# Performance work log

Measured on AMD Instinct MI355X. Metric: run time of the kernel, lower is better.

The kernel has to match this reference:

```python
import jax, jax.numpy as jnp
import numpy as np

B, S, E = 2, 2048, 1024
H, D = 16, 64
BASE = 10000.0


def rotate_half(x):
    x1, x2 = jnp.split(x, 2, axis=-1)
    return jnp.concatenate((-x2, x1), axis=-1)


def rope_cos_sin(seq_len, dim):
    inv_freq = 1.0 / (BASE ** (jnp.arange(0, dim, 2, dtype=jnp.float32) / dim))
    t = jnp.arange(seq_len, dtype=jnp.float32)
    freqs = jnp.einsum('i,j->ij', t, inv_freq)          # [S, D/2]
    emb = jnp.concatenate((freqs, freqs), axis=-1)       # [S, D]
    return jnp.cos(emb), jnp.sin(emb)


def setup_inputs() -> dict:
    key = jax.random.key(0)
    ks = jax.random.split(key, 9)
    s = 1.0 / np.sqrt(E)
    inp = {
        'x': jax.random.normal(ks[0], (B, S, E), dtype=jnp.float32),
        'mask': jnp.ones((B, S), dtype=jnp.int32),
        'Wq': jax.random.normal(ks[1], (E, H * D), dtype=jnp.float32) * s,
        'bq': jnp.zeros((H * D,), dtype=jnp.float32),
        'Wk': jax.random.normal(ks[2], (E, H * D), dtype=jnp.float32) * s,
        'bk': jnp.zeros((H * D,), dtype=jnp.float32),
        'Wv': jax.random.normal(ks[3], (E, H * D), dtype=jnp.float32) * s,
        'bv': jnp.zeros((H * D,), dtype=jnp.float32),
        'Wo': jax.random.normal(ks[4], (H * D, E), dtype=jnp.float32) * s,
        'bo': jnp.zeros((E,), dtype=jnp.float32),
    }
    return inp


def reference(x, mask, Wq, bq, Wk, bk, Wv, bv, Wo, bo):
    b, s, _ = x.shape
    scale = D ** (-0.5)
    # projections -> [B, H, S, D]
    q = (x @ Wq + bq).reshape(b, s, H, D).transpose(0, 2, 1, 3)
    k = (x @ Wk + bk).reshape(b, s, H, D).transpose(0, 2, 1, 3)
    v = (x @ Wv + bv).reshape(b, s, H, D).transpose(0, 2, 1, 3)
    # rotary position embedding
    cos, sin = rope_cos_sin(s, D)                      # [S, D]
    cos = cos[None, None]
    sin = sin[None, None]
    q = q * cos + rotate_half(q) * sin
    k = k * cos + rotate_half(k) * sin
    # scores [B, H, S, S]
    scores = jnp.einsum('bhqd,bhkd->bhqk', q, k) * scale
    # padding mask [B,1,1,S]
    scores = jnp.where(mask[:, None, None, :] == 0, -jnp.inf, scores)
    # causal mask
    i = jnp.arange(s)
    causal = jnp.where(i[None, :] > i[:, None], -jnp.inf, 0.0)  # [S, S]
    scores = scores + causal[None, None]
    attn = jax.nn.softmax(scores, axis=-1)
    ctx = jnp.einsum('bhqk,bhkd->bhqd', attn, v)
    ctx = ctx.transpose(0, 2, 1, 3).reshape(b, s, H * D)
    return ctx @ Wo + bo
```

## Files before the change

### kernel.cpp

```cpp
#include <hip/hip_runtime.h>
#include <cstdint>
#include <cstddef>

#define DEVI __device__ __forceinline__

typedef __bf16 bf16_t;
typedef __bf16 bf16x4 __attribute__((ext_vector_type(4)));
typedef __bf16 bf16x8 __attribute__((ext_vector_type(8)));
typedef float  f32x4  __attribute__((ext_vector_type(4)));
typedef float  f32x16 __attribute__((ext_vector_type(16)));
typedef unsigned short u16x4 __attribute__((ext_vector_type(4)));
typedef unsigned int   u32x4 __attribute__((ext_vector_type(4)));

static constexpr int Bz = 2, S = 2048, E = 1024, H = 16, Dh = 64;
static constexpr int M  = Bz * S;
static constexpr int N  = H * Dh;
static constexpr int Kd = E;

DEVI unsigned short f2bf(float f) {
  unsigned u = __builtin_bit_cast(unsigned, f);
  return (unsigned short)((u + 0x7fffu + ((u >> 16) & 1u)) >> 16);
}

DEVI void async_copy16(void* lds, const void* g) {
  __builtin_amdgcn_global_load_lds((__attribute__((address_space(1))) void*)(g),
                                   (__attribute__((address_space(3))) void*)(lds), 16, 0, 0);
}

DEVI void block_sync() { asm volatile("s_barrier" ::: "memory"); }
#define VMCNT4() asm volatile("s_waitcnt vmcnt(4)" ::: "memory")
#define VMCNT0() asm volatile("s_waitcnt vmcnt(0)" ::: "memory")

DEVI unsigned cvtpk(float lo, float hi) {
  unsigned r;
  asm("v_cvt_pk_bf16_f32 %0, %1, %2" : "=v"(r) : "v"(lo), "v"(hi));
  return r;
}
DEVI void swap32(unsigned& x, unsigned& y) {
  asm("v_permlane32_swap_b32 %0, %1" : "+v"(x), "+v"(y));
}

__global__ void prep_kernel(const float* __restrict__ x, bf16_t* __restrict__ xb,
                            const float* __restrict__ Wq, const float* __restrict__ Wk,
                            const float* __restrict__ Wv, const float* __restrict__ Wo,
                            bf16_t* __restrict__ WtBase,
                            float* __restrict__ ropeC, float* __restrict__ ropeS) {
  __shared__ unsigned short tile[64][68];
  const int blk = blockIdx.x, tid = threadIdx.x;
  if (blk < 4096) {
    int i = blk * 256 + tid;
    float4 v = ((const float4*)x)[i];
    u16x4 o = { f2bf(v.x), f2bf(v.y), f2bf(v.z), f2bf(v.w) };
    ((u16x4*)xb)[i] = o;
  } else if (blk < 5120) {
    const int i = blk - 4096;
    const int z = i >> 8, rest = i & 255;
    const int n0 = (rest & 15) * 64, k0 = (rest >> 4) * 64;
    const float* W = (z == 0) ? Wq : (z == 1) ? Wk : (z == 2) ? Wv : Wo;
    unsigned short* T = (unsigned short*)(WtBase + (size_t)z * Kd * N);
    for (int e = tid; e < 1024; e += 256) {
      int r = e >> 4, c4 = (e & 15) * 4;
      float4 v = *(const float4*)(W + (size_t)(k0 + r) * N + n0 + c4);
      u16x4 o = { f2bf(v.x), f2bf(v.y), f2bf(v.z), f2bf(v.w) };
      *(u16x4*)&tile[r][c4] = o;
    }
    __syncthreads();
    for (int e = tid; e < 1024; e += 256) {
      int r = e >> 4, c4 = (e & 15) * 4;
      u16x4 o = { tile[c4][r], tile[c4 + 1][r], tile[c4 + 2][r], tile[c4 + 3][r] };
      *(u16x4*)&T[(size_t)(n0 + r) * Kd + k0 + c4] = o;
    }
  } else {
    int i = (blk - 5120) * 256 + tid;
    int pos = i >> 5, j = i & 31;
    float inv = exp2f(-(float)j * 0.41524101186092029f);
    float ang = (float)pos * inv;
    ropeC[i] = cosf(ang);
    ropeS[i] = sinf(ang);
  }
}

__global__ void vtrans_kernel(const bf16_t* __restrict__ V, bf16_t* __restrict__ Vt) {
  __shared__ unsigned short tile[64][68];
  const int bh = blockIdx.y;
  const int s0 = blockIdx.x * 64;
  const unsigned short* Vp = (const unsigned short*)V + (size_t)bh * S * Dh;
  unsigned short* Tp = (unsigned short*)Vt + (size_t)bh * Dh * S;
  const int tid = threadIdx.x;
  for (int e = tid; e < 1024; e += 256) {
    int r = e >> 4, c4 = (e & 15) * 4;
    u16x4 v = *(const u16x4*)(Vp + (size_t)(s0 + r) * Dh + c4);
    *(u16x4*)&tile[r][c4] = v;
  }
  __syncthreads();
  for (int e = tid; e < 1024; e += 256) {
    int d = e >> 4, s4 = (e & 15) * 4;
    u16x4 o = { tile[s4][d], tile[s4 + 1][d], tile[s4 + 2][d], tile[s4 + 3][d] };
    *(u16x4*)&Tp[(size_t)d * S + s0 + s4] = o;
  }
}


DEVI void gemm_mainloop(const bf16_t* __restrict__ A, const bf16_t* __restrict__ Bt,
                        bf16_t* sA, bf16_t* sB, int m0, int n0, f32x4 (&acc)[4][4]) {
  const int tid  = threadIdx.x;
  const int lane = tid & 63;
  const int wid  = tid >> 6;
  const int l16  = lane & 15;
  const int quad = lane >> 4;
  const int wm = (wid >> 1) * 64;
  const int wn = (wid & 1) * 64;
  const int o0 = wid * 2048 + lane * 16;
  const int o1 = o0 + 1024;
  const int r0 = o0 >> 6, c0 = o0 & 63;
  const int r1 = o1 >> 6, c1 = o1 & 63;
  const char* Ab = (const char*)A;
  const char* Bb = (const char*)Bt;
  char* sAc = (char*)sA;
  char* sBc = (char*)sB;

  for (int k0 = 0; k0 < Kd; k0 += 32) {
    __syncthreads();
    async_copy16(sAc + wid * 2048,        Ab + ((size_t)(m0 + r0) * Kd + k0) * 2 + c0);
    async_copy16(sAc + wid * 2048 + 1024, Ab + ((size_t)(m0 + r1) * Kd + k0) * 2 + c1);
    async_copy16(sBc + wid * 2048,        Bb + ((size_t)(n0 + r0) * Kd + k0) * 2 + c0);
    async_copy16(sBc + wid * 2048 + 1024, Bb + ((size_t)(n0 + r1) * Kd + k0) * 2 + c1);
    __syncthreads();
    bf16x8 af[4], bfv[4];
#pragma unroll
    for (int mi = 0; mi < 4; ++mi)
      af[mi] = *(const bf16x8*)(sA + (wm + mi * 16 + l16) * 32 + quad * 8);
#pragma unroll
    for (int ni = 0; ni < 4; ++ni)
      bfv[ni] = *(const bf16x8*)(sB + (wn + ni * 16 + l16) * 32 + quad * 8);
#pragma unroll
    for (int mi = 0; mi < 4; ++mi)
#pragma unroll
      for (int ni = 0; ni < 4; ++ni)
        acc[mi][ni] = __builtin_amdgcn_mfma_f32_16x16x32_bf16(af[mi], bfv[ni], acc[mi][ni], 0, 0, 0);
  }
}

__global__ __launch_bounds__(256, 3) void gemm_qkv_kernel(
    const bf16_t* __restrict__ xb, const bf16_t* __restrict__ WtBase,
    const float* __restrict__ bq, const float* __restrict__ bk, const float* __restrict__ bv,
    bf16_t* __restrict__ outBase,
    const float* __restrict__ ropeC, const float* __restrict__ ropeS) {
  __shared__ bf16_t sA[4096], sB[4096];
  const int z = blockIdx.z;
  const bf16_t* Bt = WtBase + (size_t)z * Kd * N;
  const float* bias = (z == 0) ? bq : (z == 1) ? bk : bv;
  unsigned short* outp = (unsigned short*)(outBase + (size_t)z * M * N);
  const int n0 = blockIdx.x * 128, m0 = blockIdx.y * 128;
  f32x4 acc[4][4] = {};
  gemm_mainloop(xb, Bt, sA, sB, m0, n0, acc);

  const int tid = threadIdx.x, lane = tid & 63, wid = tid >> 6;
  const int l16 = lane & 15, quad = lane >> 4;
  const int wm = (wid >> 1) * 64, wn = (wid & 1) * 64;
  const int cbase = n0 + wn;
  const int h = cbase >> 6;

  if (z < 2) {
    const float qs = (z == 0) ? 0.18033688011112042f : 1.0f;
#pragma unroll
    for (int mi = 0; mi < 4; ++mi)
#pragma unroll
      for (int r = 0; r < 4; ++r) {
        int t = m0 + wm + mi * 16 + quad * 4 + r;
        int bb = t >> 11, s = t & (S - 1);
        size_t obase = ((size_t)(bb * H + h) * S + s) * Dh;
#pragma unroll
        for (int np = 0; np < 2; ++np) {
          int j = np * 16 + l16;
          float cc = ropeC[s * 32 + j];
          float ss = ropeS[s * 32 + j];
          float xlo = acc[mi][np][r]     + bias[cbase + j];
          float xhi = acc[mi][np + 2][r] + bias[cbase + j + 32];
          outp[obase + j]      = f2bf((xlo * cc - xhi * ss) * qs);
          outp[obase + j + 32] = f2bf((xhi * cc + xlo * ss) * qs);
        }
      }
  } else {
#pragma unroll
    for (int mi = 0; mi < 4; ++mi)
#pragma unroll
      for (int r = 0; r < 4; ++r) {
        int t = m0 + wm + mi * 16 + quad * 4 + r;
        int bb = t >> 11, s = t & (S - 1);
        size_t obase = ((size_t)(bb * H + h) * S + s) * Dh;
#pragma unroll
        for (int ni = 0; ni < 4; ++ni) {
          int d = ni * 16 + l16;
          outp[obase + d] = f2bf(acc[mi][ni][r] + bias[cbase + d]);
        }
      }
  }
}

__global__ __launch_bounds__(256, 4) void gemm_o_kernel(
    const bf16_t* __restrict__ A, const bf16_t* __restrict__ Bt,
    const float* __restrict__ bias, float* __restrict__ out) {
  __shared__ bf16_t sA[2048], sB[4096];
  const int n0 = blockIdx.x * 128, m0 = blockIdx.y * 64;
  const int tid = threadIdx.x, lane = tid & 63, wid = tid >> 6;
  const int l16 = lane & 15, quad = lane >> 4;
  const int wm = (wid >> 1) * 32, wn = (wid & 1) * 64;
  const int rowoff = lane >> 2, col8 = (lane & 3) * 8;
  const char* Ab = (const char*)A;
  const char* Bb = (const char*)Bt;
  char* sAc = (char*)sA;
  char* sBc = (char*)sB;
  f32x4 acc[2][4] = {};

  for (int k0 = 0; k0 < Kd; k0 += 32) {
    __syncthreads();
    async_copy16(sAc + wid * 1024,
                 Ab + ((size_t)(m0 + wid * 16 + rowoff) * Kd + k0 + col8) * 2);
    async_copy16(sBc + (wid * 2) * 1024,
                 Bb + ((size_t)(n0 + wid * 32 + rowoff) * Kd + k0 + col8) * 2);
    async_copy16(sBc + (wid * 2 + 1) * 1024,
                 Bb + ((size_t)(n0 + wid * 32 + 16 + rowoff) * Kd + k0 + col8) * 2);
    __syncthreads();
    bf16x8 af[2], bfv[4];
#pragma unroll
    for (int mi = 0; mi < 2; ++mi)
      af[mi] = *(const bf16x8*)(sA + (wm + mi * 16 + l16) * 32 + quad * 8);
#pragma unroll
    for (int ni = 0; ni < 4; ++ni)
      bfv[ni] = *(const bf16x8*)(sB + (wn + ni * 16 + l16) * 32 + quad * 8);
#pragma unroll
    for (int mi = 0; mi < 2; ++mi)
#pragma unroll
      for (int ni = 0; ni < 4; ++ni)
        acc[mi][ni] = __builtin_amdgcn_mfma_f32_16x16x32_bf16(af[mi], bfv[ni], acc[mi][ni], 0, 0, 0);
  }
#pragma unroll
  for (int mi = 0; mi < 2; ++mi)
#pragma unroll
    for (int r = 0; r < 4; ++r) {
      int t = m0 + wm + mi * 16 + quad * 4 + r;
#pragma unroll
      for (int ni = 0; ni < 4; ++ni) {
        int c = n0 + wn + ni * 16 + l16;
        out[(size_t)t * N + c] = acc[mi][ni][r] + bias[c];
      }
    }
}

template <bool MASKED>
DEVI void attn32_body(const bf16_t* __restrict__ Qp, const char* __restrict__ Kg,
                      const char* __restrict__ Vg, const int* __restrict__ mp,
                      unsigned short* __restrict__ cp, char* lds,
                      int b, int bh, int qb) {
  const int tid = threadIdx.x, lane = tid & 63, wid = tid >> 6;
  const int grp = wid >> 2, w4 = wid & 3;
  const int l32 = lane & 31, hi = lane >> 5;

  const int qw = qb * 128 + w4 * 32;
  const int qg = qw + l32;
  const int nIt = qb + 1;
  const int gk0 = grp * nIt * 64;
  char* gB = lds + grp * 32768;

  bf16x8 qf[4];
#pragma unroll
  for (int c = 0; c < 4; ++c)
    qf[c] = *(const bf16x8*)(Qp + (size_t)(qw + l32) * Dh + c * 16 + hi * 8);
  asm volatile("" :: "v"((float)qf[3][7]));

  int kLds[2], vLds[2], kOff[2], vOff[2];
#pragma unroll
  for (int i = 0; i < 2; ++i) {
    const int s = w4 * 2 + i;
    const int a = s >> 2, c = s & 3;
    kLds[i] = s * 1024;
    kOff[i] = ((a * 32 + l32) * Dh + c * 16 + hi * 8) * 2;
    vLds[i] = 8192 + s * 1024;
    vOff[i] = ((s >> 2) * 32 + l32) * (S * 2) + (((s & 3) * 16 + hi * 8) * 2);
  }

  f32x16 cacc0 = {}, cacc1 = {};
  float lsum = 0.f;

  {
    const char* ks = Kg + (size_t)gk0 * (Dh * 2);
    const char* vs = Vg + (size_t)gk0 * 2;
    async_copy16(gB + kLds[0], ks + kOff[0]);
    async_copy16(gB + kLds[1], ks + kOff[1]);
    async_copy16(gB + vLds[0], vs + vOff[0]);
    async_copy16(gB + vLds[1], vs + vOff[1]);
  }

  for (int kt = 0; kt < nIt; ++kt) {
    const int cur = kt & 1;
    const int kb = gk0 + kt * 64;
    if (kt + 1 < nIt) {
      char* dst = gB + (cur ^ 1) * 16384;
      const char* ks = Kg + (size_t)(kb + 64) * (Dh * 2);
      const char* vs = Vg + (size_t)(kb + 64) * 2;
      async_copy16(dst + kLds[0], ks + kOff[0]);
      async_copy16(dst + kLds[1], ks + kOff[1]);
      async_copy16(dst + vLds[0], vs + vOff[0]);
      async_copy16(dst + vLds[1], vs + vOff[1]);
      if (!MASKED) { VMCNT4(); }
    } else if (!MASKED) {
      VMCNT0();
    }
    unsigned long long dm = 0;
    if (MASKED) {
      int mk = mp[kb + lane];
      VMCNT0();
      dm = __ballot(mk == 0);
    }
    block_sync();

    const bf16_t* sK = (const bf16_t*)(gB + cur * 16384);
    const bf16_t* sV = (const bf16_t*)(gB + cur * 16384 + 8192);
    const bool needC = (kb + 63 > qw);

#pragma unroll
    for (int a = 0; a < 2; ++a) {
      f32x16 st = {};
      __builtin_amdgcn_s_setprio(1);
#pragma unroll
      for (int c = 0; c < 4; ++c) {
        bf16x8 kf = *(const bf16x8*)(sK + (a * 4 + c) * 512 + lane * 8);
        st = __builtin_amdgcn_mfma_f32_32x32x16_bf16(kf, qf[c], st, 0, 0, 0);
      }
      __builtin_amdgcn_s_setprio(0);
      if (MASKED && dm) {
#pragma unroll
        for (int r = 0; r < 16; ++r)
          if ((dm >> (a * 32 + (r & 3) + 8 * (r >> 2) + 4 * hi)) & 1ull) st[r] = -1e30f;
      }
      if (needC) {
        const int kbase = kb + a * 32 + 4 * hi - qg;
#pragma unroll
        for (int r = 0; r < 16; ++r)
          if (kbase + (r & 3) + 8 * (r >> 2) > 0) st[r] = -1e30f;
      }
      unsigned P0[4], P1[4];
#pragma unroll
      for (int m = 0; m < 4; ++m) {
        float p0 = exp2f(st[4 * m + 0]), p1 = exp2f(st[4 * m + 1]);
        float p2 = exp2f(st[4 * m + 2]), p3 = exp2f(st[4 * m + 3]);
        lsum += (p0 + p1) + (p2 + p3);
        P0[m] = cvtpk(p0, p1);
        P1[m] = cvtpk(p2, p3);
      }
      swap32(P0[0], P0[1]); swap32(P1[0], P1[1]);
      swap32(P0[2], P0[3]); swap32(P1[2], P1[3]);
      u32x4 t0 = { P0[0], P1[0], P0[1], P1[1] };
      u32x4 t1 = { P0[2], P1[2], P0[3], P1[3] };
      const bf16x8 f0 = __builtin_bit_cast(bf16x8, t0);
      const bf16x8 f1 = __builtin_bit_cast(bf16x8, t1);
      __builtin_amdgcn_s_setprio(1);
      {
        bf16x8 v00 = *(const bf16x8*)(sV + (0 + a * 2 + 0) * 512 + lane * 8);
        cacc0 = __builtin_amdgcn_mfma_f32_32x32x16_bf16(v00, f0, cacc0, 0, 0, 0);
        bf16x8 v01 = *(const bf16x8*)(sV + (0 + a * 2 + 1) * 512 + lane * 8);
        cacc0 = __builtin_amdgcn_mfma_f32_32x32x16_bf16(v01, f1, cacc0, 0, 0, 0);
        bf16x8 v10 = *(const bf16x8*)(sV + (4 + a * 2 + 0) * 512 + lane * 8);
        cacc1 = __builtin_amdgcn_mfma_f32_32x32x16_bf16(v10, f0, cacc1, 0, 0, 0);
        bf16x8 v11 = *(const bf16x8*)(sV + (4 + a * 2 + 1) * 512 + lane * 8);
        cacc1 = __builtin_amdgcn_mfma_f32_32x32x16_bf16(v11, f1, cacc1, 0, 0, 0);
      }
      __builtin_amdgcn_s_setprio(0);
    }
    block_sync();
  }

  float* cm = (float*)lds + (size_t)w4 * 2112;
  if (grp == 1) {
#pragma unroll
    for (int r = 0; r < 16; ++r) cm[r * 64 + lane] = cacc0[r];
#pragma unroll
    for (int r = 0; r < 16; ++r) cm[(16 + r) * 64 + lane] = cacc1[r];
    cm[2048 + lane] = lsum;
  }
  asm volatile("s_waitcnt lgkmcnt(0)" ::: "memory");
  block_sync();
  if (grp == 0) {
#pragma unroll
    for (int r = 0; r < 16; ++r) cacc0[r] += cm[r * 64 + lane];
#pragma unroll
    for (int r = 0; r < 16; ++r) cacc1[r] += cm[(16 + r) * 64 + lane];
    lsum += cm[2048 + lane];
    lsum += __shfl_xor(lsum, 32);
    const float inv = 1.0f / lsum;
    const size_t base = ((size_t)(b * S + qw + l32)) * N + (size_t)(bh & 15) * Dh;
#pragma unroll
    for (int m = 0; m < 4; ++m) {
      const int d0 = m * 8 + 4 * hi;
      u16x4 o0 = { f2bf(cacc0[4 * m + 0] * inv), f2bf(cacc0[4 * m + 1] * inv),
                   f2bf(cacc0[4 * m + 2] * inv), f2bf(cacc0[4 * m + 3] * inv) };
      *(u16x4*)&cp[base + d0] = o0;
      u16x4 o1 = { f2bf(cacc1[4 * m + 0] * inv), f2bf(cacc1[4 * m + 1] * inv),
                   f2bf(cacc1[4 * m + 2] * inv), f2bf(cacc1[4 * m + 3] * inv) };
      *(u16x4*)&cp[base + 32 + d0] = o1;
    }
  }
}

__global__ __launch_bounds__(512, 4) void attn_kernel(
    const bf16_t* __restrict__ Q, const bf16_t* __restrict__ Kb,
    const bf16_t* __restrict__ Vt, const int* __restrict__ mask,
    bf16_t* __restrict__ ctx) {
  __shared__ f32x4 ldsA[4096];

  const int idx = blockIdx.x;
  const int g  = idx >> 5;
  const int bh = idx & 31;
  const int qb = (g < 8) ? (15 - g) : (g - 8);
  const int b  = bh >> 4;
  const int lane = threadIdx.x & 63;

  const bf16_t* Qp = Q + (size_t)bh * S * Dh;
  const char*   Kg = (const char*)(Kb + (size_t)bh * S * Dh);
  const char*   Vg = (const char*)(Vt + (size_t)bh * Dh * S);
  const int*    mp = mask + b * S;

  int dead = 0;
  const int4* mp4 = (const int4*)mp;
  for (int c = lane; c < S / 4; c += 64) {
    int4 m = mp4[c];
    dead |= (m.x == 0) | (m.y == 0) | (m.z == 0) | (m.w == 0);
  }
  const bool anydead = __ballot(dead != 0) != 0ull;

  unsigned short* cp = (unsigned short*)ctx;
  if (!anydead)
    attn32_body<false>(Qp, Kg, Vg, mp, cp, (char*)ldsA, b, bh, qb);
  else
    attn32_body<true>(Qp, Kg, Vg, mp, cp, (char*)ldsA, b, bh, qb);
}


extern "C" void kernel_launch(void* const* d_in, const int* in_sizes, int n_in,
                              void* d_out, int out_size, void* d_ws, size_t ws_size,
                              hipStream_t stream) {
  const float* x  = (const float*)d_in[0];
  const int*  msk = (const int*)d_in[1];
  const float* Wq = (const float*)d_in[2];
  const float* bq = (const float*)d_in[3];
  const float* Wk = (const float*)d_in[4];
  const float* bk = (const float*)d_in[5];
  const float* Wv = (const float*)d_in[6];
  const float* bv = (const float*)d_in[7];
  const float* Wo = (const float*)d_in[8];
  const float* bo = (const float*)d_in[9];
  float* out = (float*)d_out;
  (void)in_sizes; (void)n_in; (void)out_size; (void)ws_size;

  char* ws = (char*)d_ws;
  bf16_t* xb   = (bf16_t*)(ws);
  bf16_t* WT   = (bf16_t*)(ws + (8u  << 20));
  bf16_t* qkv  = (bf16_t*)(ws + (16u << 20));
  bf16_t* Qb   = qkv;
  bf16_t* Kbuf = qkv + (size_t)1 * M * N;
  bf16_t* Vb   = qkv + (size_t)2 * M * N;
  bf16_t* Vt   = xb;
  bf16_t* ctx  = Vb;
  float* ropeC = (float*)(ws + (40u << 20));
  float* ropeS = ropeC + (size_t)S * 32;

  prep_kernel<<<5376, 256, 0, stream>>>(x, xb, Wq, Wk, Wv, Wo, WT, ropeC, ropeS);
  gemm_qkv_kernel<<<dim3(8, 32, 3), 256, 0, stream>>>(xb, WT, bq, bk, bv, qkv, ropeC, ropeS);
  vtrans_kernel<<<dim3(32, 32), 256, 0, stream>>>(Vb, Vt);
  attn_kernel<<<512, 512, 0, stream>>>(Qb, Kbuf, Vt, msk, ctx);
  gemm_o_kernel<<<dim3(8, 64), 256, 0, stream>>>(ctx, WT + (size_t)3 * Kd * N, bo, out);
}
```

Measured before the change: 196.1 us.

## Pair long and short causal query blocks per 1024-thread attention block

The attention kernel now launches 256 blocks of 1024 threads. Each block processes a long and a short causal query block in sequence (15-p then p), so the work per block is balanced. Inside each phase the key range is split across four wave groups instead of two, with uneven remainders handled by inactive iterations, and the partial accumulators from three groups are reduced through LDS with vectorized stores. This targets the causal load imbalance and tail effect. The cost is double the LDS per block, lower occupancy, extra barriers for idle groups, and a wider reduction.

```diff
diff --git a/kernel.cpp b/kernel.cpp
--- a/kernel.cpp
+++ b/kernel.cpp
@@ -249,18 +249,22 @@
 }
 
 template <bool MASKED>
-DEVI void attn32_body(const bf16_t* __restrict__ Qp, const char* __restrict__ Kg,
-                      const char* __restrict__ Vg, const int* __restrict__ mp,
-                      unsigned short* __restrict__ cp, char* lds,
-                      int b, int bh, int qb) {
+DEVI void attn32_phase(const bf16_t* __restrict__ Qp, const char* __restrict__ Kg,
+                       const char* __restrict__ Vg, const int* __restrict__ mp,
+                       unsigned short* __restrict__ cp, char* lds,
+                       int b, int bh, int qb) {
   const int tid = threadIdx.x, lane = tid & 63, wid = tid >> 6;
   const int grp = wid >> 2, w4 = wid & 3;
   const int l32 = lane & 31, hi = lane >> 5;
 
   const int qw = qb * 128 + w4 * 32;
   const int qg = qw + l32;
-  const int nIt = qb + 1;
-  const int gk0 = grp * nIt * 64;
+  const int nTot = 2 * (qb + 1);
+  const int qd = nTot >> 2, rm = nTot & 3;
+  const int nG  = qd + ((grp < rm) ? 1 : 0);
+  const int st0 = grp * qd + ((grp < rm) ? grp : rm);
+  const int nMax = qd + (rm ? 1 : 0);
+  const int gk0 = st0 * 64;
   char* gB = lds + grp * 32768;
 
   bf16x8 qf[4];
@@ -283,7 +287,7 @@
   f32x16 cacc0 = {}, cacc1 = {};
   float lsum = 0.f;
 
-  {
+  if (nG > 0) {
     const char* ks = Kg + (size_t)gk0 * (Dh * 2);
     const char* vs = Vg + (size_t)gk0 * 2;
     async_copy16(gB + kLds[0], ks + kOff[0]);
@@ -292,101 +296,124 @@
     async_copy16(gB + vLds[1], vs + vOff[1]);
   }
 
-  for (int kt = 0; kt < nIt; ++kt) {
+  for (int kt = 0; kt < nMax; ++kt) {
     const int cur = kt & 1;
     const int kb = gk0 + kt * 64;
-    if (kt + 1 < nIt) {
-      char* dst = gB + (cur ^ 1) * 16384;
-      const char* ks = Kg + (size_t)(kb + 64) * (Dh * 2);
-      const char* vs = Vg + (size_t)(kb + 64) * 2;
-      async_copy16(dst + kLds[0], ks + kOff[0]);
-      async_copy16(dst + kLds[1], ks + kOff[1]);
-      async_copy16(dst + vLds[0], vs + vOff[0]);
-      async_copy16(dst + vLds[1], vs + vOff[1]);
-      if (!MASKED) { VMCNT4(); }
-    } else if (!MASKED) {
-      VMCNT0();
-    }
+    const bool act = kt < nG;
     unsigned long long dm = 0;
-    if (MASKED) {
-      int mk = mp[kb + lane];
-      VMCNT0();
-      dm = __ballot(mk == 0);
+    if (act) {
+      if (kt + 1 < nG) {
+        char* dst = gB + (cur ^ 1) * 16384;
+        const char* ks = Kg + (size_t)(kb + 64) * (Dh * 2);
+        const char* vs = Vg + (size_t)(kb + 64) * 2;
+        async_copy16(dst + kLds[0], ks + kOff[0]);
+        async_copy16(dst + kLds[1], ks + kOff[1]);
+        async_copy16(dst + vLds[0], vs + vOff[0]);
+        async_copy16(dst + vLds[1], vs + vOff[1]);
+        if (!MASKED) { VMCNT4(); }
+      } else if (!MASKED) {
+        VMCNT0();
+      }
+      if (MASKED) {
+        int mk = mp[kb + lane];
+        VMCNT0();
+        dm = __ballot(mk == 0);
+      }
     }
     block_sync();
 
-    const bf16_t* sK = (const bf16_t*)(gB + cur * 16384);
-    const bf16_t* sV = (const bf16_t*)(gB + cur * 16384 + 8192);
-    const bool needC = (kb + 63 > qw);
-
-#pragma unroll
-    for (int a = 0; a < 2; ++a) {
-      f32x16 st = {};
-      __builtin_amdgcn_s_setprio(1);
-#pragma unroll
-      for (int c = 0; c < 4; ++c) {
-        bf16x8 kf = *(const bf16x8*)(sK + (a * 4 + c) * 512 + lane * 8);
-        st = __builtin_amdgcn_mfma_f32_32x32x16_bf16(kf, qf[c], st, 0, 0, 0);
-      }
-      __builtin_amdgcn_s_setprio(0);
-      if (MASKED && dm) {
-#pragma unroll
-        for (int r = 0; r < 16; ++r)
-          if ((dm >> (a * 32 + (r & 3) + 8 * (r >> 2) + 4 * hi)) & 1ull) st[r] = -1e30f;
-      }
-      if (needC) {
-        const int kbase = kb + a * 32 + 4 * hi - qg;
-#pragma unroll
-        for (int r = 0; r < 16; ++r)
-          if (kbase + (r & 3) + 8 * (r >> 2) > 0) st[r] = -1e30f;
-      }
-      unsigned P0[4], P1[4];
-#pragma unroll
-      for (int m = 0; m < 4; ++m) {
-        float p0 = exp2f(st[4 * m + 0]), p1 = exp2f(st[4 * m + 1]);
-        float p2 = exp2f(st[4 * m + 2]), p3 = exp2f(st[4 * m + 3]);
-        lsum += (p0 + p1) + (p2 + p3);
-        P0[m] = cvtpk(p0, p1);
-        P1[m] = cvtpk(p2, p3);
-      }
-      swap32(P0[0], P0[1]); swap32(P1[0], P1[1]);
-      swap32(P0[2], P0[3]); swap32(P1[2], P1[3]);
-      u32x4 t0 = { P0[0], P1[0], P0[1], P1[1] };
-      u32x4 t1 = { P0[2], P1[2], P0[3], P1[3] };
-      const bf16x8 f0 = __builtin_bit_cast(bf16x8, t0);
-      const bf16x8 f1 = __builtin_bit_cast(bf16x8, t1);
-      __builtin_amdgcn_s_setprio(1);
-      {
-        bf16x8 v00 = *(const bf16x8*)(sV + (0 + a * 2 + 0) * 512 + lane * 8);
-        cacc0 = __builtin_amdgcn_mfma_f32_32x32x16_bf16(v00, f0, cacc0, 0, 0, 0);
-        bf16x8 v01 = *(const bf16x8*)(sV + (0 + a * 2 + 1) * 512 + lane * 8);
-        cacc0 = __builtin_amdgcn_mfma_f32_32x32x16_bf16(v01, f1, cacc0, 0, 0, 0);
-        bf16x8 v10 = *(const bf16x8*)(sV + (4 + a * 2 + 0) * 512 + lane * 8);
-        cacc1 = __builtin_amdgcn_mfma_f32_32x32x16_bf16(v10, f0, cacc1, 0, 0, 0);
-        bf16x8 v11 = *(const bf16x8*)(sV + (4 + a * 2 + 1) * 512 + lane * 8);
-        cacc1 = __builtin_amdgcn_mfma_f32_32x32x16_bf16(v11, f1, cacc1, 0, 0, 0);
-      }
-      __builtin_amdgcn_s_setprio(0);
+    if (act) {
+      const bf16_t* sK = (const bf16_t*)(gB + cur * 16384);
+      const bf16_t* sV = (const bf16_t*)(gB + cur * 16384 + 8192);
+      const bool needC = (kb + 63 > qw);
+
+#pragma unroll
+      for (int a = 0; a < 2; ++a) {
+        f32x16 st = {};
+        __builtin_amdgcn_s_setprio(1);
+#pragma unroll
+        for (int c = 0; c < 4; ++c) {
+          bf16x8 kf = *(const bf16x8*)(sK + (a * 4 + c) * 512 + lane * 8);
+          st = __builtin_amdgcn_mfma_f32_32x32x16_bf16(kf, qf[c], st, 0, 0, 0);
+        }
+        __builtin_amdgcn_s_setprio(0);
+        if (MASKED && dm) {
+#pragma unroll
+          for (int r = 0; r < 16; ++r)
+            if ((dm >> (a * 32 + (r & 3) + 8 * (r >> 2) + 4 * hi)) & 1ull) st[r] = -1e30f;
+        }
+        if (needC) {
+          const int kbase = kb + a * 32 + 4 * hi - qg;
+#pragma unroll
+          for (int r = 0; r < 16; ++r)
+            if (kbase + (r & 3) + 8 * (r >> 2) > 0) st[r] = -1e30f;
+        }
+        unsigned P0[4], P1[4];
+#pragma unroll
+        for (int m = 0; m < 4; ++m) {
+          float p0 = exp2f(st[4 * m + 0]), p1 = exp2f(st[4 * m + 1]);
+          float p2 = exp2f(st[4 * m + 2]), p3 = exp2f(st[4 * m + 3]);
+          lsum += (p0 + p1) + (p2 + p3);
+          P0[m] = cvtpk(p0, p1);
+          P1[m] = cvtpk(p2, p3);
+        }
+        swap32(P0[0], P0[1]); swap32(P1[0], P1[1]);
+        swap32(P0[2], P0[3]); swap32(P1[2], P1[3]);
+        u32x4 t0 = { P0[0], P1[0], P0[1], P1[1] };
+        u32x4 t1 = { P0[2], P1[2], P0[3], P1[3] };
+        const bf16x8 f0 = __builtin_bit_cast(bf16x8, t0);
+        const bf16x8 f1 = __builtin_bit_cast(bf16x8, t1);
+        __builtin_amdgcn_s_setprio(1);
+        {
+          bf16x8 v00 = *(const bf16x8*)(sV + (0 + a * 2 + 0) * 512 + lane * 8);
+          cacc0 = __builtin_amdgcn_mfma_f32_32x32x16_bf16(v00, f0, cacc0, 0, 0, 0);
+          bf16x8 v01 = *(const bf16x8*)(sV + (0 + a * 2 + 1) * 512 + lane * 8);
+          cacc0 = __builtin_amdgcn_mfma_f32_32x32x16_bf16(v01, f1, cacc0, 0, 0, 0);
+          bf16x8 v10 = *(const bf16x8*)(sV + (4 + a * 2 + 0) * 512 + lane * 8);
+          cacc1 = __builtin_amdgcn_mfma_f32_32x32x16_bf16(v10, f0, cacc1, 0, 0, 0);
+          bf16x8 v11 = *(const bf16x8*)(sV + (4 + a * 2 + 1) * 512 + lane * 8);
+          cacc1 = __builtin_amdgcn_mfma_f32_32x32x16_bf16(v11, f1, cacc1, 0, 0, 0);
+        }
+        __builtin_amdgcn_s_setprio(0);
+      }
     }
     block_sync();
   }
 
-  float* cm = (float*)lds + (size_t)w4 * 2112;
-  if (grp == 1) {
-#pragma unroll
-    for (int r = 0; r < 16; ++r) cm[r * 64 + lane] = cacc0[r];
-#pragma unroll
-    for (int r = 0; r < 16; ++r) cm[(16 + r) * 64 + lane] = cacc1[r];
-    cm[2048 + lane] = lsum;
+  if (grp != 0) {
+    char* rb = lds + (size_t)((grp - 1) * 4 + w4) * 8448;
+#pragma unroll
+    for (int c = 0; c < 4; ++c) {
+      f32x4 v = { cacc0[4 * c], cacc0[4 * c + 1], cacc0[4 * c + 2], cacc0[4 * c + 3] };
+      *(f32x4*)(rb + c * 1024 + lane * 16) = v;
+    }
+#pragma unroll
+    for (int c = 0; c < 4; ++c) {
+      f32x4 v = { cacc1[4 * c], cacc1[4 * c + 1], cacc1[4 * c + 2], cacc1[4 * c + 3] };
+      *(f32x4*)(rb + (4 + c) * 1024 + lane * 16) = v;
+    }
+    *(float*)(rb + 8192 + lane * 4) = lsum;
   }
   asm volatile("s_waitcnt lgkmcnt(0)" ::: "memory");
   block_sync();
   if (grp == 0) {
 #pragma unroll
-    for (int r = 0; r < 16; ++r) cacc0[r] += cm[r * 64 + lane];
-#pragma unroll
-    for (int r = 0; r < 16; ++r) cacc1[r] += cm[(16 + r) * 64 + lane];
-    lsum += cm[2048 + lane];
+    for (int j = 1; j < 4; ++j) {
+      const char* rb = lds + (size_t)((j - 1) * 4 + w4) * 8448;
+#pragma unroll
+      for (int c = 0; c < 4; ++c) {
+        f32x4 v = *(const f32x4*)(rb + c * 1024 + lane * 16);
+        cacc0[4 * c] += v[0]; cacc0[4 * c + 1] += v[1];
+        cacc0[4 * c + 2] += v[2]; cacc0[4 * c + 3] += v[3];
+      }
+#pragma unroll
+      for (int c = 0; c < 4; ++c) {
+        f32x4 v = *(const f32x4*)(rb + (4 + c) * 1024 + lane * 16);
+        cacc1[4 * c] += v[0]; cacc1[4 * c + 1] += v[1];
+        cacc1[4 * c + 2] += v[2]; cacc1[4 * c + 3] += v[3];
+      }
+      lsum += *(const float*)(rb + 8192 + lane * 4);
+    }
     lsum += __shfl_xor(lsum, 32);
     const float inv = 1.0f / lsum;
     const size_t base = ((size_t)(b * S + qw + l32)) * N + (size_t)(bh & 15) * Dh;
@@ -401,19 +428,20 @@
       *(u16x4*)&cp[base + 32 + d0] = o1;
     }
   }
-}
-
-__global__ __launch_bounds__(512, 4) void attn_kernel(
+  block_sync();
+}
+
+__global__ __launch_bounds__(1024, 4) void attn_kernel(
     const bf16_t* __restrict__ Q, const bf16_t* __restrict__ Kb,
     const bf16_t* __restrict__ Vt, const int* __restrict__ mask,
     bf16_t* __restrict__ ctx) {
-  __shared__ f32x4 ldsA[4096];
+  __shared__ f32x4 ldsbuf[8192];
 
   const int idx = blockIdx.x;
-  const int g  = idx >> 5;
-  const int bh = idx & 31;
-  const int qb = (g < 8) ? (15 - g) : (g - 8);
-  const int b  = bh >> 4;
+  const int p   = idx >> 5;
+  const int bh  = idx & 31;
+  const int qbL = 15 - p, qbS = p;
+  const int b   = bh >> 4;
   const int lane = threadIdx.x & 63;
 
   const bf16_t* Qp = Q + (size_t)bh * S * Dh;
@@ -430,10 +458,16 @@
   const bool anydead = __ballot(dead != 0) != 0ull;
 
   unsigned short* cp = (unsigned short*)ctx;
-  if (!anydead)
-    attn32_body<false>(Qp, Kg, Vg, mp, cp, (char*)ldsA, b, bh, qb);
-  else
-    attn32_body<true>(Qp, Kg, Vg, mp, cp, (char*)ldsA, b, bh, qb);
+  char* lds = (char*)ldsbuf;
+  if (!anydead) {
+#pragma unroll 1
+    for (int t = 0; t < 2; ++t)
+      attn32_phase<false>(Qp, Kg, Vg, mp, cp, lds, b, bh, t ? qbS : qbL);
+  } else {
+#pragma unroll 1
+    for (int t = 0; t < 2; ++t)
+      attn32_phase<true>(Qp, Kg, Vg, mp, cp, lds, b, bh, t ? qbS : qbL);
+  }
 }
 
 
@@ -468,6 +502,6 @@
   prep_kernel<<<5376, 256, 0, stream>>>(x, xb, Wq, Wk, Wv, Wo, WT, ropeC, ropeS);
   gemm_qkv_kernel<<<dim3(8, 32, 3), 256, 0, stream>>>(xb, WT, bq, bk, bv, qkv, ropeC, ropeS);
   vtrans_kernel<<<dim3(32, 32), 256, 0, stream>>>(Vb, Vt);
-  attn_kernel<<<512, 512, 0, stream>>>(Qb, Kbuf, Vt, msk, ctx);
+  attn_kernel<<<256, 1024, 0, stream>>>(Qb, Kbuf, Vt, msk, ctx);
   gemm_o_kernel<<<dim3(8, 64), 256, 0, stream>>>(ctx, WT + (size_t)3 * Kd * N, bo, out);
 }
```

Result: slower. 224.2 us (+14.3%).

## Store V transposed in 32-key tiles and refine causal masking and combine

Applied to the files above, without the earlier changes.

The V-transpose kernel now writes V^T in contiguous 32-key blocks ([tile][d][32]), so each 64-key chunk is one contiguous 8 KB region. The attention loader then treats K and V uniformly: each warp issues four 16-byte async copies from a single source, replacing strided row loads of V^T. The causal mask is now checked per 32-key half instead of per 64-key chunk, which skips masking work on more sub-tiles. The cross-group accumulator combine uses vectorized f32x4 LDS stores and loads with a rotated index to spread banks, and the lsum shuffle moves before the exchange.

```diff
diff --git a/kernel.cpp b/kernel.cpp
--- a/kernel.cpp
+++ b/kernel.cpp
@@ -30,6 +30,7 @@
 DEVI void block_sync() { asm volatile("s_barrier" ::: "memory"); }
 #define VMCNT4() asm volatile("s_waitcnt vmcnt(4)" ::: "memory")
 #define VMCNT0() asm volatile("s_waitcnt vmcnt(0)" ::: "memory")
+#define LGKM0()  asm volatile("s_waitcnt lgkmcnt(0)" ::: "memory")
 
 DEVI unsigned cvtpk(float lo, float hi) {
   unsigned r;
@@ -85,7 +86,7 @@
   const int bh = blockIdx.y;
   const int s0 = blockIdx.x * 64;
   const unsigned short* Vp = (const unsigned short*)V + (size_t)bh * S * Dh;
-  unsigned short* Tp = (unsigned short*)Vt + (size_t)bh * Dh * S;
+  unsigned short* Tp = (unsigned short*)Vt + (size_t)bh * S * Dh;
   const int tid = threadIdx.x;
   for (int e = tid; e < 1024; e += 256) {
     int r = e >> 4, c4 = (e & 15) * 4;
@@ -95,8 +96,9 @@
   __syncthreads();
   for (int e = tid; e < 1024; e += 256) {
     int d = e >> 4, s4 = (e & 15) * 4;
+    int t = (s0 + s4) >> 5, ks = (s0 + s4) & 31;
     u16x4 o = { tile[s4][d], tile[s4 + 1][d], tile[s4 + 2][d], tile[s4 + 3][d] };
-    *(u16x4*)&Tp[(size_t)d * S + s0 + s4] = o;
+    *(u16x4*)&Tp[((size_t)t * Dh + d) * 32 + ks] = o;
   }
 }
 
@@ -249,17 +251,17 @@
 }
 
 template <bool MASKED>
-DEVI void attn32_body(const bf16_t* __restrict__ Qp, const char* __restrict__ Kg,
+DEVI void attn32_tile(const bf16_t* __restrict__ Qp, const char* __restrict__ Kg,
                       const char* __restrict__ Vg, const int* __restrict__ mp,
                       unsigned short* __restrict__ cp, char* lds,
-                      int b, int bh, int qb) {
+                      int b, int bh, int j) {
   const int tid = threadIdx.x, lane = tid & 63, wid = tid >> 6;
   const int grp = wid >> 2, w4 = wid & 3;
   const int l32 = lane & 31, hi = lane >> 5;
 
-  const int qw = qb * 128 + w4 * 32;
+  const int qw = j * 128 + w4 * 32;
   const int qg = qw + l32;
-  const int nIt = qb + 1;
+  const int nIt = j + 1;
   const int gk0 = grp * nIt * 64;
   char* gB = lds + grp * 32768;
 
@@ -269,45 +271,43 @@
     qf[c] = *(const bf16x8*)(Qp + (size_t)(qw + l32) * Dh + c * 16 + hi * 8);
   asm volatile("" :: "v"((float)qf[3][7]));
 
-  int kLds[2], vLds[2], kOff[2], vOff[2];
-#pragma unroll
-  for (int i = 0; i < 2; ++i) {
-    const int s = w4 * 2 + i;
-    const int a = s >> 2, c = s & 3;
-    kLds[i] = s * 1024;
-    kOff[i] = ((a * 32 + l32) * Dh + c * 16 + hi * 8) * 2;
-    vLds[i] = 8192 + s * 1024;
-    vOff[i] = ((s >> 2) * 32 + l32) * (S * 2) + (((s & 3) * 16 + hi * 8) * 2);
-  }
+  int sLds[4], sOff[4];
+#pragma unroll
+  for (int i = 0; i < 4; ++i) {
+    const int s = w4 * 4 + i;
+    sLds[i] = s * 1024;
+    if (s < 8) {
+      const int a = s >> 2, c = s & 3;
+      sOff[i] = (a * 32 + l32) * 128 + c * 32 + hi * 16;
+    } else {
+      const int t = s - 8, a = t >> 2, v = t & 3;
+      sOff[i] = a * 4096 + ((v >> 1) * 32 + l32) * 64 + (v & 1) * 32 + hi * 16;
+    }
+  }
+  const char* gsrc = (w4 < 2) ? Kg : Vg;
 
   f32x16 cacc0 = {}, cacc1 = {};
   float lsum = 0.f;
 
   {
-    const char* ks = Kg + (size_t)gk0 * (Dh * 2);
-    const char* vs = Vg + (size_t)gk0 * 2;
-    async_copy16(gB + kLds[0], ks + kOff[0]);
-    async_copy16(gB + kLds[1], ks + kOff[1]);
-    async_copy16(gB + vLds[0], vs + vOff[0]);
-    async_copy16(gB + vLds[1], vs + vOff[1]);
+    const char* bp = gsrc + (size_t)gk0 * 128;
+#pragma unroll
+    for (int i = 0; i < 4; ++i) async_copy16(gB + sLds[i], bp + sOff[i]);
   }
 
   for (int kt = 0; kt < nIt; ++kt) {
     const int cur = kt & 1;
     const int kb = gk0 + kt * 64;
+    unsigned long long dm = 0;
     if (kt + 1 < nIt) {
+      const char* bp = gsrc + (size_t)(kb + 64) * 128;
       char* dst = gB + (cur ^ 1) * 16384;
-      const char* ks = Kg + (size_t)(kb + 64) * (Dh * 2);
-      const char* vs = Vg + (size_t)(kb + 64) * 2;
-      async_copy16(dst + kLds[0], ks + kOff[0]);
-      async_copy16(dst + kLds[1], ks + kOff[1]);
-      async_copy16(dst + vLds[0], vs + vOff[0]);
-      async_copy16(dst + vLds[1], vs + vOff[1]);
+#pragma unroll
+      for (int i = 0; i < 4; ++i) async_copy16(dst + sLds[i], bp + sOff[i]);
       if (!MASKED) { VMCNT4(); }
     } else if (!MASKED) {
       VMCNT0();
     }
-    unsigned long long dm = 0;
     if (MASKED) {
       int mk = mp[kb + lane];
       VMCNT0();
@@ -315,17 +315,14 @@
     }
     block_sync();
 
-    const bf16_t* sK = (const bf16_t*)(gB + cur * 16384);
-    const bf16_t* sV = (const bf16_t*)(gB + cur * 16384 + 8192);
-    const bool needC = (kb + 63 > qw);
-
+    const bf16_t* sT = (const bf16_t*)(gB + cur * 16384);
 #pragma unroll
     for (int a = 0; a < 2; ++a) {
       f32x16 st = {};
       __builtin_amdgcn_s_setprio(1);
 #pragma unroll
       for (int c = 0; c < 4; ++c) {
-        bf16x8 kf = *(const bf16x8*)(sK + (a * 4 + c) * 512 + lane * 8);
+        bf16x8 kf = *(const bf16x8*)(sT + a * 2048 + c * 512 + lane * 8);
         st = __builtin_amdgcn_mfma_f32_32x32x16_bf16(kf, qf[c], st, 0, 0, 0);
       }
       __builtin_amdgcn_s_setprio(0);
@@ -334,8 +331,9 @@
         for (int r = 0; r < 16; ++r)
           if ((dm >> (a * 32 + (r & 3) + 8 * (r >> 2) + 4 * hi)) & 1ull) st[r] = -1e30f;
       }
-      if (needC) {
-        const int kbase = kb + a * 32 + 4 * hi - qg;
+      const int kba = kb + a * 32;
+      if (kba + 31 > qw) {
+        const int kbase = kba + 4 * hi - qg;
 #pragma unroll
         for (int r = 0; r < 16; ++r)
           if (kbase + (r & 3) + 8 * (r >> 2) > 0) st[r] = -1e30f;
@@ -357,13 +355,13 @@
       const bf16x8 f1 = __builtin_bit_cast(bf16x8, t1);
       __builtin_amdgcn_s_setprio(1);
       {
-        bf16x8 v00 = *(const bf16x8*)(sV + (0 + a * 2 + 0) * 512 + lane * 8);
+        bf16x8 v00 = *(const bf16x8*)(sT + 4096 + a * 2048 + 0 * 512 + lane * 8);
         cacc0 = __builtin_amdgcn_mfma_f32_32x32x16_bf16(v00, f0, cacc0, 0, 0, 0);
-        bf16x8 v01 = *(const bf16x8*)(sV + (0 + a * 2 + 1) * 512 + lane * 8);
+        bf16x8 v01 = *(const bf16x8*)(sT + 4096 + a * 2048 + 1 * 512 + lane * 8);
         cacc0 = __builtin_amdgcn_mfma_f32_32x32x16_bf16(v01, f1, cacc0, 0, 0, 0);
-        bf16x8 v10 = *(const bf16x8*)(sV + (4 + a * 2 + 0) * 512 + lane * 8);
+        bf16x8 v10 = *(const bf16x8*)(sT + 4096 + a * 2048 + 2 * 512 + lane * 8);
         cacc1 = __builtin_amdgcn_mfma_f32_32x32x16_bf16(v10, f0, cacc1, 0, 0, 0);
-        bf16x8 v11 = *(const bf16x8*)(sV + (4 + a * 2 + 1) * 512 + lane * 8);
+        bf16x8 v11 = *(const bf16x8*)(sT + 4096 + a * 2048 + 3 * 512 + lane * 8);
         cacc1 = __builtin_amdgcn_mfma_f32_32x32x16_bf16(v11, f1, cacc1, 0, 0, 0);
       }
       __builtin_amdgcn_s_setprio(0);
@@ -371,24 +369,39 @@
     block_sync();
   }
 
-  float* cm = (float*)lds + (size_t)w4 * 2112;
+  lsum += __shfl_xor(lsum, 32);
+  float* reg = (float*)lds;
   if (grp == 1) {
-#pragma unroll
-    for (int r = 0; r < 16; ++r) cm[r * 64 + lane] = cacc0[r];
-#pragma unroll
-    for (int r = 0; r < 16; ++r) cm[(16 + r) * 64 + lane] = cacc1[r];
-    cm[2048 + lane] = lsum;
-  }
-  asm volatile("s_waitcnt lgkmcnt(0)" ::: "memory");
+    float* rb = reg + w4 * 2048 + l32 * 64;
+#pragma unroll
+    for (int m = 0; m < 4; ++m) {
+      f32x4 v = { cacc0[4 * m], cacc0[4 * m + 1], cacc0[4 * m + 2], cacc0[4 * m + 3] };
+      *(f32x4*)(rb + ((8 * m + 4 * hi + 4 * l32) & 63)) = v;
+    }
+#pragma unroll
+    for (int m = 0; m < 4; ++m) {
+      f32x4 v = { cacc1[4 * m], cacc1[4 * m + 1], cacc1[4 * m + 2], cacc1[4 * m + 3] };
+      *(f32x4*)(rb + ((32 + 8 * m + 4 * hi + 4 * l32) & 63)) = v;
+    }
+    reg[8192 + w4 * 32 + l32] = lsum;
+  }
+  LGKM0();
   block_sync();
   if (grp == 0) {
-#pragma unroll
-    for (int r = 0; r < 16; ++r) cacc0[r] += cm[r * 64 + lane];
-#pragma unroll
-    for (int r = 0; r < 16; ++r) cacc1[r] += cm[(16 + r) * 64 + lane];
-    lsum += cm[2048 + lane];
-    lsum += __shfl_xor(lsum, 32);
-    const float inv = 1.0f / lsum;
+    const float* rb = reg + w4 * 2048 + l32 * 64;
+#pragma unroll
+    for (int m = 0; m < 4; ++m) {
+      f32x4 v = *(const f32x4*)(rb + ((8 * m + 4 * hi + 4 * l32) & 63));
+      cacc0[4 * m] += v[0]; cacc0[4 * m + 1] += v[1];
+      cacc0[4 * m + 2] += v[2]; cacc0[4 * m + 3] += v[3];
+    }
+#pragma unroll
+    for (int m = 0; m < 4; ++m) {
+      f32x4 v = *(const f32x4*)(rb + ((32 + 8 * m + 4 * hi + 4 * l32) & 63));
+      cacc1[4 * m] += v[0]; cacc1[4 * m + 1] += v[1];
+      cacc1[4 * m + 2] += v[2]; cacc1[4 * m + 3] += v[3];
+    }
+    const float inv = 1.0f / (lsum + reg[8192 + w4 * 32 + l32]);
     const size_t base = ((size_t)(b * S + qw + l32)) * N + (size_t)(bh & 15) * Dh;
 #pragma unroll
     for (int m = 0; m < 4; ++m) {
@@ -407,18 +420,18 @@
     const bf16_t* __restrict__ Q, const bf16_t* __restrict__ Kb,
     const bf16_t* __restrict__ Vt, const int* __restrict__ mask,
     bf16_t* __restrict__ ctx) {
-  __shared__ f32x4 ldsA[4096];
+  __shared__ f32x4 ldsbuf[4096];
 
   const int idx = blockIdx.x;
-  const int g  = idx >> 5;
-  const int bh = idx & 31;
-  const int qb = (g < 8) ? (15 - g) : (g - 8);
-  const int b  = bh >> 4;
+  const int t   = idx >> 5;
+  const int j   = (t < 8) ? (15 - t) : (t - 8);
+  const int bh  = idx & 31;
+  const int b   = bh >> 4;
   const int lane = threadIdx.x & 63;
 
   const bf16_t* Qp = Q + (size_t)bh * S * Dh;
   const char*   Kg = (const char*)(Kb + (size_t)bh * S * Dh);
-  const char*   Vg = (const char*)(Vt + (size_t)bh * Dh * S);
+  const char*   Vg = (const char*)(Vt + (size_t)bh * S * Dh);
   const int*    mp = mask + b * S;
 
   int dead = 0;
@@ -430,10 +443,11 @@
   const bool anydead = __ballot(dead != 0) != 0ull;
 
   unsigned short* cp = (unsigned short*)ctx;
+  char* lds = (char*)ldsbuf;
   if (!anydead)
-    attn32_body<false>(Qp, Kg, Vg, mp, cp, (char*)ldsA, b, bh, qb);
+    attn32_tile<false>(Qp, Kg, Vg, mp, cp, lds, b, bh, j);
   else
-    attn32_body<true>(Qp, Kg, Vg, mp, cp, (char*)ldsA, b, bh, qb);
+    attn32_tile<true>(Qp, Kg, Vg, mp, cp, lds, b, bh, j);
 }
 
 
```

After: 194.0 us. About the same (-1.1%).
